# Optimization experiments

Hardware: AMD Instinct MI355X
Metric: run time of the kernel (lower is better)

The kernel has to match this reference:

```python
import jax, jax.numpy as jnp
import numpy as np
from math import comb

DEGREE = 3


def build_index_tables(n, degree):
    """For each degree d in [2, degree], build (first, rest) int arrays so that
    row_d = x[first] * row_{d-1}[rest], where row_d lists the values of all
    ordered (multiset) degree-d monomials in lexicographic order.
    An ordered d-tuple starting with i has its tail t[1:] being an ordered
    (d-1)-tuple with elements in [i, n); in lexicographic order these occupy
    the tail of row_{d-1}, starting at prev_len - comb(n-i+d-2, d-1)."""
    tables = []
    prev_len = n  # row_1 = x itself
    for d in range(2, degree + 1):
        starts = np.array([prev_len - comb(n - i + d - 2, d - 1) for i in range(n)], dtype=np.int64)
        rest = np.concatenate([np.arange(s, prev_len, dtype=np.int32) for s in starts])
        first = np.repeat(np.arange(n, dtype=np.int32), prev_len - starts)
        tables.append((jnp.asarray(first), jnp.asarray(rest)))
        prev_len = rest.shape[0]
    return tables


def setup_inputs() -> dict:
    key = jax.random.key(0)
    n, out_size = 256, 32
    ks = jax.random.split(key, 5)
    sizes = [comb(n + d - 1, d) for d in range(DEGREE + 1)]  # [1, 256, 32896, 2829056]
    inp = {"x": jax.random.normal(ks[0], (n,), dtype=jnp.float32)}
    for d in range(DEGREE + 1):
        fan_in = sizes[d]
        bound = 1.0 / np.sqrt(fan_in)  # kaiming_uniform with a=sqrt(5)
        inp[f"coeff_deg_{d}"] = jax.random.uniform(
            ks[d + 1], (out_size, fan_in), dtype=jnp.float32, minval=-bound, maxval=bound)
    return inp


def reference(x, coeff_deg_0, coeff_deg_1, coeff_deg_2, coeff_deg_3):
    n = x.shape[0]
    tables = build_index_tables(n, DEGREE)  # static numpy work at trace time
    rows = [jnp.ones((1,), dtype=x.dtype), x]
    for first, rest in tables:
        rows.append(x[first] * rows[-1][rest])  # gather + elementwise product
    coeffs = [coeff_deg_0, coeff_deg_1, coeff_deg_2, coeff_deg_3]
    out = coeffs[0] @ rows[0]
    for c, r in zip(coeffs[1:], rows[1:]):
        out = out + c @ r  # (out_size, m_d) @ (m_d,) -> (out_size,)
    return out
```

## Files before the change

kernel.cpp:

```cpp
#include <hip/hip_runtime.h>

constexpr int N   = 256;
constexpr int OUT = 32;
constexpr int OPG = 8;
constexpr int OG  = OUT / OPG;
constexpr int M2  = 32896;
constexpr int M3  = 2829056;
constexpr int Q3  = M3 / 4;
constexpr int Q2  = M2 / 4;
constexpr int B3  = 691;
constexpr int B2  = 33;
constexpr int BX  = B3 + B2;

__device__ __forceinline__ int c3_tail(int s) {
    return s * (s + 1) * (s + 2) / 6;
}

__global__ __launch_bounds__(256) void poly_partial(
    const float* __restrict__ x, const float* __restrict__ c2,
    const float* __restrict__ c3, float* __restrict__ partial)
{
    __shared__ float xs[N];
    const int tid = threadIdx.x;
    if (tid < N) xs[tid] = x[tid];
    __syncthreads();

    const int g     = blockIdx.y;
    const int obase = g * OPG;

    float acc[OPG];
#pragma unroll
    for (int oo = 0; oo < OPG; ++oo) acc[oo] = 0.f;

    if ((int)blockIdx.x < B3) {
        for (int it = 0; it < 4; ++it) {
            const int q = (int)blockIdx.x * 256 + tid + it * (B3 * 256);
            if (q >= Q3) break;
            const int base = q * 4;

            int lo = 0, hi = N - 1;
            while (lo < hi) {
                int mid = (lo + hi + 1) >> 1;
                int O = M3 - c3_tail(N - mid);
                if (O <= base) lo = mid; else hi = mid - 1;
            }
            const int i = lo;
            const int s = N - i;
            const int rem = base - (M3 - c3_tail(s));
            lo = 0; hi = s - 1;
            while (lo < hi) {
                int mid = (lo + hi + 1) >> 1;
                int A = mid * s - (mid * (mid - 1)) / 2;
                if (A <= rem) lo = mid; else hi = mid - 1;
            }
            const int a = lo;
            int j = i + a, k = j + (rem - (a * s - (a * (a - 1)) / 2));
            int ii = i;

            float v[4];
#pragma unroll
            for (int t = 0; t < 4; ++t) {
                v[t] = xs[ii] * xs[j] * xs[k];
                ++k;
                if (k == N) { ++j; if (j == N) { ++ii; j = ii; } k = j; }
            }
            const float* p = c3 + (size_t)obase * M3 + base;
#pragma unroll
            for (int oo = 0; oo < OPG; ++oo) {
                const float4 c = *reinterpret_cast<const float4*>(p + (size_t)oo * M3);
                acc[oo] += c.x * v[0] + c.y * v[1] + c.z * v[2] + c.w * v[3];
            }
        }
    } else {
        const int q = ((int)blockIdx.x - B3) * 256 + tid;
        if (q < Q2) {
            const int base = q * 4;
            int lo = 0, hi = N - 1;
            while (lo < hi) {
                int mid = (lo + hi + 1) >> 1;
                int O = mid * N - (mid * (mid - 1)) / 2;
                if (O <= base) lo = mid; else hi = mid - 1;
            }
            int j = lo;
            int k = j + (base - (j * N - (j * (j - 1)) / 2));
            float v[4];
#pragma unroll
            for (int t = 0; t < 4; ++t) {
                v[t] = xs[j] * xs[k];
                ++k;
                if (k == N) { ++j; k = j; }
            }
            const float* p = c2 + (size_t)obase * M2 + base;
#pragma unroll
            for (int oo = 0; oo < OPG; ++oo) {
                const float4 c = *reinterpret_cast<const float4*>(p + (size_t)oo * M2);
                acc[oo] += c.x * v[0] + c.y * v[1] + c.z * v[2] + c.w * v[3];
            }
        }
    }

    __shared__ float red[4][OPG];
    const int lane = tid & 63, wid = tid >> 6;
#pragma unroll
    for (int oo = 0; oo < OPG; ++oo) {
        float a = acc[oo];
#pragma unroll
        for (int off = 32; off > 0; off >>= 1) a += __shfl_down(a, off);
        if (lane == 0) red[wid][oo] = a;
    }
    __syncthreads();
    if (tid < OPG) {
        partial[((size_t)g * BX + blockIdx.x) * OPG + tid] =
            red[0][tid] + red[1][tid] + red[2][tid] + red[3][tid];
    }
}

__global__ __launch_bounds__(1024) void poly_final(
    const float* __restrict__ partial, const float* __restrict__ x,
    const float* __restrict__ c0, const float* __restrict__ c1,
    float* __restrict__ out)
{
    __shared__ float lds[1024];
    const int tid = threadIdx.x;
    const int o = tid & 31, c = tid >> 5;
    const int g = o >> 3, oo = o & 7;

    float a = 0.f;
    for (int b = c; b < BX; b += 32)
        a += partial[((size_t)g * BX + b) * OPG + oo];
#pragma unroll
    for (int e = 0; e < 8; ++e) {
        const int k = c * 8 + e;
        a += c1[o * N + k] * x[k];
    }
    if (c == 0) a += c0[o];
    lds[tid] = a;
    __syncthreads();
    if (tid < 32) {
        float s = 0.f;
#pragma unroll
        for (int cc = 0; cc < 32; ++cc) s += lds[cc * 32 + tid];
        out[tid] = s;
    }
}

extern "C" void kernel_launch(void* const* d_in, const int* in_sizes, int n_in,
                              void* d_out, int out_size, void* d_ws, size_t ws_size,
                              hipStream_t stream) {
    const float* x  = (const float*)d_in[0];
    const float* c0 = (const float*)d_in[1];
    const float* c1 = (const float*)d_in[2];
    const float* c2 = (const float*)d_in[3];
    const float* c3 = (const float*)d_in[4];
    float* out     = (float*)d_out;
    float* partial = (float*)d_ws;

    dim3 grid(BX, OG);
    poly_partial<<<grid, 256, 0, stream>>>(x, c2, c3, partial);
    poly_final<<<1, 1024, 0, stream>>>(partial, x, c0, c1, out);
}
```

Baseline: 81.10 us.

## Use persistent 256-block grid with non-temporal coefficient loads

Replaces the 724x4 grid, where each block did up to 4 iterations, with a 256x4 grid in which every block loops 11 times over the degree-3 coefficients. The degree-2 work is folded into the last 48 blocks as a tail. Coefficient reads become non-temporal float4 loads, a min-blocks launch bound is added, and the final reduction loop is unrolled. The goal is better load balance with one block per CU slot and less cache pollution from the streaming reads. The cost is fewer blocks in flight, which may hide memory latency less well, and the degree-2 tail adds some imbalance.

```diff
diff --git a/kernel.cpp b/kernel.cpp
--- a/kernel.cpp
+++ b/kernel.cpp
@@ -8,15 +8,17 @@
 constexpr int M3  = 2829056;
 constexpr int Q3  = M3 / 4;
 constexpr int Q2  = M2 / 4;
-constexpr int B3  = 691;
-constexpr int B2  = 33;
-constexpr int BX  = B3 + B2;
+constexpr int BX  = 256;
+constexpr int IT3 = 11;
+constexpr int D2_FIRST = 208;
+
+typedef float f32x4 __attribute__((ext_vector_type(4)));
 
 __device__ __forceinline__ int c3_tail(int s) {
     return s * (s + 1) * (s + 2) / 6;
 }
 
-__global__ __launch_bounds__(256) void poly_partial(
+__global__ __launch_bounds__(256, 4) void poly_partial(
     const float* __restrict__ x, const float* __restrict__ c2,
     const float* __restrict__ c3, float* __restrict__ partial)
 {
@@ -25,19 +27,19 @@
     if (tid < N) xs[tid] = x[tid];
     __syncthreads();
 
-    const int g     = blockIdx.y;
-    const int obase = g * OPG;
+    const int bx = blockIdx.x;
+    const int g  = blockIdx.y;
 
     float acc[OPG];
 #pragma unroll
     for (int oo = 0; oo < OPG; ++oo) acc[oo] = 0.f;
 
-    if ((int)blockIdx.x < B3) {
-        for (int it = 0; it < 4; ++it) {
-            const int q = (int)blockIdx.x * 256 + tid + it * (B3 * 256);
-            if (q >= Q3) break;
+    const float* __restrict__ c3g = c3 + (size_t)g * OPG * M3;
+
+    for (int it = 0; it < IT3; ++it) {
+        const int q = bx * 256 + tid + it * (BX * 256);
+        if (q < Q3) {
             const int base = q * 4;
-
             int lo = 0, hi = N - 1;
             while (lo < hi) {
                 int mid = (lo + hi + 1) >> 1;
@@ -54,8 +56,7 @@
                 if (A <= rem) lo = mid; else hi = mid - 1;
             }
             const int a = lo;
-            int j = i + a, k = j + (rem - (a * s - (a * (a - 1)) / 2));
-            int ii = i;
+            int ii = i, j = i + a, k = j + (rem - (a * s - (a * (a - 1)) / 2));
 
             float v[4];
 #pragma unroll
@@ -64,15 +65,18 @@
                 ++k;
                 if (k == N) { ++j; if (j == N) { ++ii; j = ii; } k = j; }
             }
-            const float* p = c3 + (size_t)obase * M3 + base;
+            const float* p = c3g + base;
 #pragma unroll
             for (int oo = 0; oo < OPG; ++oo) {
-                const float4 c = *reinterpret_cast<const float4*>(p + (size_t)oo * M3);
-                acc[oo] += c.x * v[0] + c.y * v[1] + c.z * v[2] + c.w * v[3];
+                const f32x4 c = __builtin_nontemporal_load(
+                    reinterpret_cast<const f32x4*>(p + (size_t)oo * M3));
+                acc[oo] += c[0] * v[0] + c[1] * v[1] + c[2] * v[2] + c[3] * v[3];
             }
         }
-    } else {
-        const int q = ((int)blockIdx.x - B3) * 256 + tid;
+    }
+
+    if (bx >= D2_FIRST) {
+        const int q = (bx - D2_FIRST) * 256 + tid;
         if (q < Q2) {
             const int base = q * 4;
             int lo = 0, hi = N - 1;
@@ -90,11 +94,12 @@
                 ++k;
                 if (k == N) { ++j; k = j; }
             }
-            const float* p = c2 + (size_t)obase * M2 + base;
+            const float* p = c2 + (size_t)g * OPG * M2 + base;
 #pragma unroll
             for (int oo = 0; oo < OPG; ++oo) {
-                const float4 c = *reinterpret_cast<const float4*>(p + (size_t)oo * M2);
-                acc[oo] += c.x * v[0] + c.y * v[1] + c.z * v[2] + c.w * v[3];
+                const f32x4 c = __builtin_nontemporal_load(
+                    reinterpret_cast<const f32x4*>(p + (size_t)oo * M2));
+                acc[oo] += c[0] * v[0] + c[1] * v[1] + c[2] * v[2] + c[3] * v[3];
             }
         }
     }
@@ -110,7 +115,7 @@
     }
     __syncthreads();
     if (tid < OPG) {
-        partial[((size_t)g * BX + blockIdx.x) * OPG + tid] =
+        partial[((size_t)g * BX + bx) * OPG + tid] =
             red[0][tid] + red[1][tid] + red[2][tid] + red[3][tid];
     }
 }
@@ -126,8 +131,11 @@
     const int g = o >> 3, oo = o & 7;
 
     float a = 0.f;
-    for (int b = c; b < BX; b += 32)
+#pragma unroll
+    for (int r = 0; r < BX / 32; ++r) {
+        const int b = c + r * 32;
         a += partial[((size_t)g * BX + b) * OPG + oo];
+    }
 #pragma unroll
     for (int e = 0; e < 8; ++e) {
         const int k = c * 8 + e;
```

Result: faster. 69.41 us (-14.4%).
